# Kernel tuning notes

Hardware: AMD Instinct MI355X
Metric: run time of the kernel (lower is better)

Reference implementation:

```python
import jax, jax.numpy as jnp
import numpy as np

N_NODES = 100000
NUM_REL = 2


def rgcn_conv(x, src, dst, etype, W, root, bias):
    """PyG-style RGCNConv: per-relation mean aggregation + root transform + bias.
    x: [N, in], W: [R, in, out], root: [in, out], bias: [out].
    """
    R = W.shape[0]
    N = x.shape[0]
    # Pre-transform nodes by every relation weight: [R, N, out]
    xr = jnp.einsum('ni,rio->rno', x, W)
    msgs = xr[etype, src]  # [E, out] gather per-edge, relation-typed
    seg_id = dst * R + etype  # combined (node, relation) segment id
    summed = jax.ops.segment_sum(msgs, seg_id, num_segments=N * R)
    cnt = jax.ops.segment_sum(jnp.ones(etype.shape, x.dtype), seg_id, num_segments=N * R)
    summed = summed.reshape(N, R, -1)
    cnt = cnt.reshape(N, R, 1)
    agg = (summed / jnp.maximum(cnt, 1.0)).sum(axis=1)  # sum over relations of per-relation means
    return agg + x @ root + bias


def setup_inputs() -> dict:
    key = jax.random.key(0)
    ks = jax.random.split(key, 9)
    d = 128
    E = 800000
    sc = 1.0 / np.sqrt(d)
    return {
        'x': jax.random.normal(ks[0], (N_NODES, d), jnp.float32),
        'edge_index_a': jax.random.randint(ks[1], (2, E), 0, N_NODES, jnp.int64),
        'edge_index_b': jax.random.randint(ks[2], (2, E), 0, N_NODES, jnp.int64),
        'W1': jax.random.normal(ks[3], (NUM_REL, d, d), jnp.float32) * sc,
        'root1': jax.random.normal(ks[4], (d, d), jnp.float32) * sc,
        'b1': jnp.zeros((d,), jnp.float32),
        'W2': jax.random.normal(ks[5], (NUM_REL, d, d), jnp.float32) * sc,
        'root2': jax.random.normal(ks[6], (d, d), jnp.float32) * sc,
        'b2': jnp.zeros((d,), jnp.float32),
    }


def reference(x, edge_index_a, edge_index_b, W1, root1, b1, W2, root2, b2):
    # Concatenate per-relation edge lists + build edge_type ids (a->0, b->1)
    edge_index = jnp.concatenate([edge_index_a, edge_index_b], axis=1)
    etype = jnp.concatenate([
        jnp.zeros((edge_index_a.shape[1],), jnp.int32),
        jnp.ones((edge_index_b.shape[1],), jnp.int32),
    ])
    src, dst = edge_index[0], edge_index[1]
    h = rgcn_conv(x, src, dst, etype, W1, root1, b1)
    h = jax.nn.relu(h)
    out = rgcn_conv(h, src, dst, etype, W2, root2, b2)
    return out
```

## Files before the change

kernel.cpp:

```cpp
#include <hip/hip_runtime.h>
#include <hip/hip_bf16.h>


typedef __attribute__((ext_vector_type(8))) short bf16x8;
typedef __attribute__((ext_vector_type(4))) float f32x4;
typedef unsigned short ushort_t;
typedef unsigned int uint_t;

#define BSHIFT 9
#define SEGB (1 << (BSHIFT + 1))
#define NBMAX 256
#define SLAB 16384
#define CH_PER_THREAD 8
#define CHUNK (256 * CH_PER_THREAD)

#define GBM 256
#define KCH 128
#define LDBE 136

#define ROWB 768
#define XOFF 512

__device__ __forceinline__ ushort_t f2b(float f) {
  union { float f; uint_t u; } v;
  v.f = f;
  uint_t u = v.u;
  return (ushort_t)((u + 0x7FFFu + ((u >> 16) & 1u)) >> 16);
}
__device__ __forceinline__ void dot2acc(float& a, uint_t pk, uint_t sel) {
  asm("v_dot2_f32_bf16 %0, %1, %2, %0" : "+v"(a) : "v"(pk), "v"(sel));
}

__global__ __launch_bounds__(256) void prep(
    const float* __restrict__ W1, const float* __restrict__ root1,
    const float* __restrict__ W2, const float* __restrict__ root2,
    ushort_t* __restrict__ Bt1, ushort_t* __restrict__ Bt2,
    const float* __restrict__ x, ushort_t* __restrict__ aggbuf1, int N) {
  int b = blockIdx.x;
  if (b < 384) {
    int flat = b * 256 + threadIdx.x;
    int which = flat >= 49152;
    int idx = flat - which * 49152;
    int c = idx / 384;
    int k = idx - c * 384;
    const float* W = which ? W2 : W1;
    const float* root = which ? root2 : root1;
    ushort_t* Bt = which ? Bt2 : Bt1;
    float v = (k < 256) ? W[(size_t)k * 128 + c] : root[(size_t)(k - 256) * 128 + c];
    Bt[(size_t)c * 384 + k] = f2b(v);
  } else {
    int idx = (b - 384) * 256 + threadIdx.x;
    int n = idx >> 6, lane = idx & 63;
    if (n < N) {
      float2 v = *(const float2*)(x + (size_t)n * 128 + lane * 2);
      uint_t pk = (uint_t)f2b(v.x) | ((uint_t)f2b(v.y) << 16);
      *(uint_t*)(aggbuf1 + (size_t)n * 384 + 256 + lane * 2) = pk;
    }
  }
}

__global__ __launch_bounds__(256) void bucket_bin(
    const int* __restrict__ ea, const int* __restrict__ eb,
    int E, int NB, int* __restrict__ cursor, uint_t* __restrict__ staging) {
  __shared__ int h[NBMAX];
  __shared__ int bbase[NBMAX];
  __shared__ int lofs[NBMAX];
  __shared__ int sscan[256];
  __shared__ uint_t sval[CHUNK];
  __shared__ int sdst[CHUNK];
  int t = threadIdx.x;
  for (int i = t; i < NB; i += 256) h[i] = 0;
  __syncthreads();

  int tbase = blockIdx.x * CHUNK + t;
  int total = 2 * E;
  uint_t val[CH_PER_THREAD];
  short bktv[CH_PER_THREAD];
#pragma unroll
  for (int j = 0; j < CH_PER_THREAD; ++j) {
    int i = tbase + j * 256;
    if (i < total) {
      int src, dst, rel;
      if (i < E) { src = ea[i];     dst = ea[E + i]; rel = 0; }
      else       { src = eb[i - E]; dst = eb[i];     rel = 1; }
      int seg = dst * 2 + rel;
      int bkt = seg >> (BSHIFT + 1);
      val[j] = ((uint_t)src << 10) | (uint_t)(seg & (SEGB - 1));
      bktv[j] = (short)bkt;
      atomicAdd(&h[bkt], 1);
    } else {
      bktv[j] = -1;
    }
  }
  __syncthreads();
  {
    int v = (t < NB) ? h[t] : 0;
    sscan[t] = v;
    __syncthreads();
    for (int off = 1; off < 256; off <<= 1) {
      int tmp = (t >= off) ? sscan[t - off] : 0;
      __syncthreads();
      sscan[t] += tmp;
      __syncthreads();
    }
    if (t < NB) {
      lofs[t] = sscan[t] - v;
      bbase[t] = v ? t * SLAB + atomicAdd(&cursor[t], v) : 0;
    }
  }
  __syncthreads();
  for (int i = t; i < NB; i += 256) h[i] = 0;
  __syncthreads();
#pragma unroll
  for (int j = 0; j < CH_PER_THREAD; ++j) {
    if (bktv[j] >= 0) {
      int bkt = bktv[j];
      int r = atomicAdd(&h[bkt], 1);
      int pos = lofs[bkt] + r;
      sval[pos] = val[j];
      sdst[pos] = bbase[bkt] + r;
    }
  }
  __syncthreads();
  int nrec = total - blockIdx.x * CHUNK;
  if (nrec > CHUNK) nrec = CHUNK;
  for (int i = t; i < nrec; i += 256)
    staging[sdst[i]] = sval[i];
}

__global__ __launch_bounds__(256) void bucket_build(
    const uint_t* __restrict__ staging, const int* __restrict__ cursor,
    int* __restrict__ csr, int* __restrict__ offs,
    int* __restrict__ ends, int nseg) {
  __shared__ int scnt[SEGB];
  __shared__ int sexcl[SEGB];
  __shared__ int sdata[256];
  int b = blockIdx.x;
  int t = threadIdx.x;
  int base = b * SLAB;
  int ne = cursor[b];
  int seg0 = b << (BSHIFT + 1);

  for (int i = t; i < SEGB; i += 256) scnt[i] = 0;
  __syncthreads();
  const uint_t* st = staging + base;
  for (int i = t; i < ne; i += 256) {
    atomicAdd(&scnt[st[i] & (SEGB - 1)], 1);
  }
  __syncthreads();
  int c0 = scnt[t * 4 + 0], c1 = scnt[t * 4 + 1];
  int c2 = scnt[t * 4 + 2], c3 = scnt[t * 4 + 3];
  int s = c0 + c1 + c2 + c3;
  sdata[t] = s;
  __syncthreads();
  for (int off = 1; off < 256; off <<= 1) {
    int tmp = (t >= off) ? sdata[t - off] : 0;
    __syncthreads();
    sdata[t] += tmp;
    __syncthreads();
  }
  int excl = sdata[t] - s;
  int e0 = excl, e1 = excl + c0, e2 = e1 + c1, e3 = e2 + c2;
  sexcl[t * 4 + 0] = e0;
  sexcl[t * 4 + 1] = e1;
  sexcl[t * 4 + 2] = e2;
  sexcl[t * 4 + 3] = e3;
  {
    int g = seg0 + t * 4;
    if (g + 0 < nseg) { offs[g + 0] = base + e0; ends[g + 0] = base + e0 + c0; }
    if (g + 1 < nseg) { offs[g + 1] = base + e1; ends[g + 1] = base + e1 + c1; }
    if (g + 2 < nseg) { offs[g + 2] = base + e2; ends[g + 2] = base + e2 + c2; }
    if (g + 3 < nseg) { offs[g + 3] = base + e3; ends[g + 3] = base + e3 + c3; }
  }
  scnt[t * 4 + 0] = 0;
  scnt[t * 4 + 1] = 0;
  scnt[t * 4 + 2] = 0;
  scnt[t * 4 + 3] = 0;
  __syncthreads();
  for (int i = t; i < ne; i += 256) {
    uint_t rec = st[i];
    int seg = (int)(rec & (SEGB - 1));
    int src = (int)(rec >> 10);
    int r = atomicAdd(&scnt[seg], 1);
    csr[base + sexcl[seg] + r] = src * ROWB + XOFF;
  }
}

__global__ __launch_bounds__(256) void agg_kernel(
    const char* __restrict__ xbc,
    const int* __restrict__ csr,
    const int* __restrict__ offs, const int* __restrict__ ends,
    ushort_t* __restrict__ agg, int nseg) {
  int wid = (blockIdx.x * blockDim.x + threadIdx.x) >> 6;
  if (wid >= nseg) return;
  int lane = threadIdx.x & 63;
  int q = lane >> 4;
  int t = lane & 15;
  int beg = offs[wid], end = ends[wid];
  const uint_t sel_lo = 0x00003F80u;
  const uint_t sel_hi = 0x3F800000u;

  float acc[8];
#pragma unroll
  for (int j = 0; j < 8; ++j) acc[j] = 0.f;

  const char* xt = xbc + t * 16;
  int e = beg + q;
  for (; e + 4 < end; e += 8) {
    int o0 = csr[e];
    int o1 = csr[e + 4];
    uint4 v0 = *(const uint4*)(xt + o0);
    uint4 v1 = *(const uint4*)(xt + o1);
    dot2acc(acc[0], v0.x, sel_lo); dot2acc(acc[1], v0.x, sel_hi);
    dot2acc(acc[2], v0.y, sel_lo); dot2acc(acc[3], v0.y, sel_hi);
    dot2acc(acc[4], v0.z, sel_lo); dot2acc(acc[5], v0.z, sel_hi);
    dot2acc(acc[6], v0.w, sel_lo); dot2acc(acc[7], v0.w, sel_hi);
    dot2acc(acc[0], v1.x, sel_lo); dot2acc(acc[1], v1.x, sel_hi);
    dot2acc(acc[2], v1.y, sel_lo); dot2acc(acc[3], v1.y, sel_hi);
    dot2acc(acc[4], v1.z, sel_lo); dot2acc(acc[5], v1.z, sel_hi);
    dot2acc(acc[6], v1.w, sel_lo); dot2acc(acc[7], v1.w, sel_hi);
  }
  if (e < end) {
    int o0 = csr[e];
    uint4 v0 = *(const uint4*)(xt + o0);
    dot2acc(acc[0], v0.x, sel_lo); dot2acc(acc[1], v0.x, sel_hi);
    dot2acc(acc[2], v0.y, sel_lo); dot2acc(acc[3], v0.y, sel_hi);
    dot2acc(acc[4], v0.z, sel_lo); dot2acc(acc[5], v0.z, sel_hi);
    dot2acc(acc[6], v0.w, sel_lo); dot2acc(acc[7], v0.w, sel_hi);
  }

#pragma unroll
  for (int j = 0; j < 8; ++j) {
    acc[j] += __shfl_xor(acc[j], 16);
    acc[j] += __shfl_xor(acc[j], 32);
  }

  int c = end - beg;
  float inv = 1.0f / (float)(c > 1 ? c : 1);
  if (q == 0) {
    uint4 o;
    o.x = (uint_t)f2b(acc[0] * inv) | ((uint_t)f2b(acc[1] * inv) << 16);
    o.y = (uint_t)f2b(acc[2] * inv) | ((uint_t)f2b(acc[3] * inv) << 16);
    o.z = (uint_t)f2b(acc[4] * inv) | ((uint_t)f2b(acc[5] * inv) << 16);
    o.w = (uint_t)f2b(acc[6] * inv) | ((uint_t)f2b(acc[7] * inv) << 16);
    int n = wid >> 1, r = wid & 1;
    *(uint4*)(agg + (size_t)n * 384 + r * 128 + t * 8) = o;
  }
}

__device__ __forceinline__ void do_mfma32(
    const char* bs, f32x4 (&acc)[4][8], const bf16x8 (&a)[4],
    int ks, int lrow, int kg) {
  bf16x8 b[8];
#pragma unroll
  for (int c = 0; c < 8; ++c)
    b[c] = *(const bf16x8*)(bs + (c * 16 + lrow) * (LDBE * 2) +
                            (ks * 4 + kg) * 16);
#pragma unroll
  for (int r = 0; r < 4; ++r)
#pragma unroll
    for (int c = 0; c < 8; ++c)
      acc[r][c] = __builtin_amdgcn_mfma_f32_16x16x32_bf16(a[r], b[c], acc[r][c], 0, 0, 0);
}

template <int MODE>
__global__ __launch_bounds__(256, 2) void mfma_gemm(
    const ushort_t* __restrict__ A,
    const ushort_t* __restrict__ Bt,
    const float* __restrict__ bias,
    float* __restrict__ outf,
    ushort_t* __restrict__ outb,
    int M) {
  __shared__ __align__(16) ushort_t Bs[2][128 * LDBE];
  const int tid = threadIdx.x;
  const int lane = tid & 63;
  const int wave = tid >> 6;
  const int lrow = lane & 15;
  const int kg = lane >> 4;
  const int rowbase = blockIdx.x * GBM + wave * 64;

  f32x4 acc[4][8];
#pragma unroll
  for (int r = 0; r < 4; ++r)
#pragma unroll
    for (int c = 0; c < 8; ++c) acc[r][c] = (f32x4){0.f, 0.f, 0.f, 0.f};

  uint4 stg[8];
#pragma unroll
  for (int j = 0; j < 8; ++j) {
    int flat = tid + j * 256;
    int col = flat >> 4;
    int q = flat & 15;
    stg[j] = *(const uint4*)(Bt + (size_t)col * 384 + q * 8);
  }
#pragma unroll
  for (int j = 0; j < 8; ++j) {
    int flat = tid + j * 256;
    int col = flat >> 4;
    int q = flat & 15;
    *(uint4*)((char*)&Bs[0][0] + col * (LDBE * 2) + q * 16) = stg[j];
  }
  __syncthreads();

  int cur = 0;
  for (int ch = 0; ch < 3; ++ch) {
    if (ch < 2) {
#pragma unroll
      for (int j = 0; j < 8; ++j) {
        int flat = tid + j * 256;
        int col = flat >> 4;
        int q = flat & 15;
        stg[j] = *(const uint4*)(Bt + (size_t)col * 384 + (ch + 1) * KCH + q * 8);
      }
    }
    const ushort_t* ab = A + (size_t)ch * KCH + kg * 8;
    const char* bsbase = (const char*)&Bs[0][0] + cur * (128 * LDBE * 2);
    bf16x8 aA[4], aB[4];
#pragma unroll
    for (int r = 0; r < 4; ++r)
      aA[r] = *(const bf16x8*)(ab + (size_t)(rowbase + r * 16 + lrow) * 384);
#pragma unroll
    for (int r = 0; r < 4; ++r)
      aB[r] = *(const bf16x8*)(ab + (size_t)(rowbase + r * 16 + lrow) * 384 + 32);
    do_mfma32(bsbase, acc, aA, 0, lrow, kg);
#pragma unroll
    for (int r = 0; r < 4; ++r)
      aA[r] = *(const bf16x8*)(ab + (size_t)(rowbase + r * 16 + lrow) * 384 + 64);
    do_mfma32(bsbase, acc, aB, 1, lrow, kg);
#pragma unroll
    for (int r = 0; r < 4; ++r)
      aB[r] = *(const bf16x8*)(ab + (size_t)(rowbase + r * 16 + lrow) * 384 + 96);
    do_mfma32(bsbase, acc, aA, 2, lrow, kg);
    do_mfma32(bsbase, acc, aB, 3, lrow, kg);
    if (ch < 2) {
#pragma unroll
      for (int j = 0; j < 8; ++j) {
        int flat = tid + j * 256;
        int col = flat >> 4;
        int q = flat & 15;
        *(uint4*)((char*)&Bs[0][0] + (cur ^ 1) * (128 * LDBE * 2) +
                  col * (LDBE * 2) + q * 16) = stg[j];
      }
      __syncthreads();
      cur ^= 1;
    }
  }

  if (MODE == 1) {
    __syncthreads();
    ushort_t* ws = (ushort_t*)&Bs[0][0] + wave * (64 * 128);
#pragma unroll
    for (int c = 0; c < 8; ++c) {
      int col = c * 16 + lrow;
      float bv = bias[col];
#pragma unroll
      for (int r = 0; r < 4; ++r)
#pragma unroll
        for (int j = 0; j < 4; ++j) {
          float v = fmaxf(acc[r][c][j] + bv, 0.f);
          ws[(r * 16 + kg * 4 + j) * 128 + col] = f2b(v);
        }
    }
    __syncthreads();
#pragma unroll
    for (int rr = 0; rr < 16; ++rr) {
      int lr = rr * 4 + (lane >> 4);
      int row = rowbase + lr;
      int tq = lane & 15;
      if (row < M) {
        uint4 v = *(const uint4*)(ws + lr * 128 + tq * 8);
        *(uint4*)(outb + (size_t)row * 384 + 256 + tq * 8) = v;
      }
    }
  } else {
#pragma unroll
    for (int c = 0; c < 8; ++c) {
      int col = c * 16 + lrow;
      float bv = bias[col];
#pragma unroll
      for (int r = 0; r < 4; ++r) {
        int r0 = rowbase + r * 16 + kg * 4;
#pragma unroll
        for (int j = 0; j < 4; ++j) {
          int row = r0 + j;
          if (row < M) {
            outf[(size_t)row * 128 + col] = acc[r][c][j] + bv;
          }
        }
      }
    }
  }
}

extern "C" void kernel_launch(void* const* d_in, const int* in_sizes, int n_in,
                              void* d_out, int out_size, void* d_ws, size_t ws_size,
                              hipStream_t stream) {
  const float* x     = (const float*)d_in[0];
  const int*   ea    = (const int*)d_in[1];
  const int*   eb    = (const int*)d_in[2];
  const float* W1    = (const float*)d_in[3];
  const float* root1 = (const float*)d_in[4];
  const float* b1    = (const float*)d_in[5];
  const float* W2    = (const float*)d_in[6];
  const float* root2 = (const float*)d_in[7];
  const float* b2    = (const float*)d_in[8];
  float* out = (float*)d_out;

  const int N = in_sizes[0] / 128;
  const int E = in_sizes[1] / 2;
  const int nseg = N * 2;
  const int Mblk = (N + GBM - 1) / GBM;
  const int Mpad = Mblk * GBM;
  const int NB = ((N - 1) >> BSHIFT) + 1;
  const int nchunk = (2 * E + CHUNK - 1) / CHUNK;
  const int XSB = (N * 64 + 255) / 256;

  char* p = (char*)d_ws;
  ushort_t* aggbuf1 = (ushort_t*)p;  p += (size_t)Mpad * 384 * sizeof(ushort_t);
  ushort_t* aggbuf2 = (ushort_t*)p;  p += (size_t)Mpad * 384 * sizeof(ushort_t);
  ushort_t* Bt1 = (ushort_t*)p;      p += (size_t)128 * 384 * sizeof(ushort_t);
  ushort_t* Bt2 = (ushort_t*)p;      p += (size_t)128 * 384 * sizeof(ushort_t);
  int* csr = (int*)p;                p += (size_t)NBMAX * SLAB * sizeof(int);
  int* offs = (int*)p;               p += (size_t)nseg * sizeof(int);
  int* ends = (int*)p;               p += (size_t)nseg * sizeof(int);
  int* cursor = (int*)p;             p += NBMAX * sizeof(int);
  uint_t* staging = (uint_t*)aggbuf2;

  hipMemsetAsync(cursor, 0, NBMAX * sizeof(int), stream);

  prep<<<384 + XSB, 256, 0, stream>>>(
      W1, root1, W2, root2, Bt1, Bt2, x, aggbuf1, N);

  bucket_bin<<<nchunk, 256, 0, stream>>>(ea, eb, E, NB, cursor, staging);
  bucket_build<<<NB, 256, 0, stream>>>(staging, cursor, csr, offs, ends, nseg);

  const int agg_blocks = (nseg + 3) / 4;

  agg_kernel<<<agg_blocks, 256, 0, stream>>>((const char*)aggbuf1, csr, offs,
                                             ends, aggbuf1, nseg);
  mfma_gemm<1><<<Mblk, 256, 0, stream>>>(aggbuf1, Bt1, b1, nullptr, aggbuf2, N);

  agg_kernel<<<agg_blocks, 256, 0, stream>>>((const char*)aggbuf2, csr, offs,
                                             ends, aggbuf2, nseg);
  mfma_gemm<0><<<Mblk, 256, 0, stream>>>(aggbuf2, Bt2, b2, out, nullptr, N);
}
```

Baseline: 308.0 us.

## Fuse edge binning into prep kernel and widen bucket_build to 1024 threads

```diff
diff --git a/kernel.cpp b/kernel.cpp
--- a/kernel.cpp
+++ b/kernel.cpp
@@ -31,14 +31,81 @@
   asm("v_dot2_f32_bf16 %0, %1, %2, %0" : "+v"(a) : "v"(pk), "v"(sel));
 }
 
-__global__ __launch_bounds__(256) void prep(
+__global__ __launch_bounds__(256) void prep_bin(
+    const int* __restrict__ ea, const int* __restrict__ eb, int E, int NB,
+    int* __restrict__ cursor, uint_t* __restrict__ staging, int nchunk,
     const float* __restrict__ W1, const float* __restrict__ root1,
     const float* __restrict__ W2, const float* __restrict__ root2,
     ushort_t* __restrict__ Bt1, ushort_t* __restrict__ Bt2,
     const float* __restrict__ x, ushort_t* __restrict__ aggbuf1, int N) {
+  __shared__ int h[NBMAX];
+  __shared__ int bbase[NBMAX];
+  __shared__ int lofs[NBMAX];
+  __shared__ int sscan[256];
+  __shared__ uint_t sval[CHUNK];
+  __shared__ int sdst[CHUNK];
   int b = blockIdx.x;
-  if (b < 384) {
-    int flat = b * 256 + threadIdx.x;
+  int t = threadIdx.x;
+
+  if (b < nchunk) {
+    for (int i = t; i < NB; i += 256) h[i] = 0;
+    __syncthreads();
+    int tbase = b * CHUNK + t;
+    int total = 2 * E;
+    uint_t val[CH_PER_THREAD];
+    short bktv[CH_PER_THREAD];
+#pragma unroll
+    for (int j = 0; j < CH_PER_THREAD; ++j) {
+      int i = tbase + j * 256;
+      if (i < total) {
+        int src, dst, rel;
+        if (i < E) { src = ea[i];     dst = ea[E + i]; rel = 0; }
+        else       { src = eb[i - E]; dst = eb[i];     rel = 1; }
+        int seg = dst * 2 + rel;
+        int bkt = seg >> (BSHIFT + 1);
+        val[j] = ((uint_t)src << 10) | (uint_t)(seg & (SEGB - 1));
+        bktv[j] = (short)bkt;
+        atomicAdd(&h[bkt], 1);
+      } else {
+        bktv[j] = -1;
+      }
+    }
+    __syncthreads();
+    {
+      int v = (t < NB) ? h[t] : 0;
+      sscan[t] = v;
+      __syncthreads();
+      for (int off = 1; off < 256; off <<= 1) {
+        int tmp = (t >= off) ? sscan[t - off] : 0;
+        __syncthreads();
+        sscan[t] += tmp;
+        __syncthreads();
+      }
+      if (t < NB) {
+        lofs[t] = sscan[t] - v;
+        bbase[t] = v ? t * SLAB + atomicAdd(&cursor[t], v) : 0;
+      }
+    }
+    __syncthreads();
+    for (int i = t; i < NB; i += 256) h[i] = 0;
+    __syncthreads();
+#pragma unroll
+    for (int j = 0; j < CH_PER_THREAD; ++j) {
+      if (bktv[j] >= 0) {
+        int bkt = bktv[j];
+        int r = atomicAdd(&h[bkt], 1);
+        int pos = lofs[bkt] + r;
+        sval[pos] = val[j];
+        sdst[pos] = bbase[bkt] + r;
+      }
+    }
+    __syncthreads();
+    int nrec = 2 * E - b * CHUNK;
+    if (nrec > CHUNK) nrec = CHUNK;
+    for (int i = t; i < nrec; i += 256)
+      staging[sdst[i]] = sval[i];
+  } else if (b < nchunk + 384) {
+    int flat = (b - nchunk) * 256 + t;
     int which = flat >= 49152;
     int idx = flat - which * 49152;
     int c = idx / 384;
@@ -49,7 +116,7 @@
     float v = (k < 256) ? W[(size_t)k * 128 + c] : root[(size_t)(k - 256) * 128 + c];
     Bt[(size_t)c * 384 + k] = f2b(v);
   } else {
-    int idx = (b - 384) * 256 + threadIdx.x;
+    int idx = (b - nchunk - 384) * 256 + t;
     int n = idx >> 6, lane = idx & 63;
     if (n < N) {
       float2 v = *(const float2*)(x + (size_t)n * 128 + lane * 2);
@@ -59,125 +126,43 @@
   }
 }
 
-__global__ __launch_bounds__(256) void bucket_bin(
-    const int* __restrict__ ea, const int* __restrict__ eb,
-    int E, int NB, int* __restrict__ cursor, uint_t* __restrict__ staging) {
-  __shared__ int h[NBMAX];
-  __shared__ int bbase[NBMAX];
-  __shared__ int lofs[NBMAX];
-  __shared__ int sscan[256];
-  __shared__ uint_t sval[CHUNK];
-  __shared__ int sdst[CHUNK];
-  int t = threadIdx.x;
-  for (int i = t; i < NB; i += 256) h[i] = 0;
-  __syncthreads();
-
-  int tbase = blockIdx.x * CHUNK + t;
-  int total = 2 * E;
-  uint_t val[CH_PER_THREAD];
-  short bktv[CH_PER_THREAD];
-#pragma unroll
-  for (int j = 0; j < CH_PER_THREAD; ++j) {
-    int i = tbase + j * 256;
-    if (i < total) {
-      int src, dst, rel;
-      if (i < E) { src = ea[i];     dst = ea[E + i]; rel = 0; }
-      else       { src = eb[i - E]; dst = eb[i];     rel = 1; }
-      int seg = dst * 2 + rel;
-      int bkt = seg >> (BSHIFT + 1);
-      val[j] = ((uint_t)src << 10) | (uint_t)(seg & (SEGB - 1));
-      bktv[j] = (short)bkt;
-      atomicAdd(&h[bkt], 1);
-    } else {
-      bktv[j] = -1;
-    }
-  }
-  __syncthreads();
-  {
-    int v = (t < NB) ? h[t] : 0;
-    sscan[t] = v;
-    __syncthreads();
-    for (int off = 1; off < 256; off <<= 1) {
-      int tmp = (t >= off) ? sscan[t - off] : 0;
-      __syncthreads();
-      sscan[t] += tmp;
-      __syncthreads();
-    }
-    if (t < NB) {
-      lofs[t] = sscan[t] - v;
-      bbase[t] = v ? t * SLAB + atomicAdd(&cursor[t], v) : 0;
-    }
-  }
-  __syncthreads();
-  for (int i = t; i < NB; i += 256) h[i] = 0;
-  __syncthreads();
-#pragma unroll
-  for (int j = 0; j < CH_PER_THREAD; ++j) {
-    if (bktv[j] >= 0) {
-      int bkt = bktv[j];
-      int r = atomicAdd(&h[bkt], 1);
-      int pos = lofs[bkt] + r;
-      sval[pos] = val[j];
-      sdst[pos] = bbase[bkt] + r;
-    }
-  }
-  __syncthreads();
-  int nrec = total - blockIdx.x * CHUNK;
-  if (nrec > CHUNK) nrec = CHUNK;
-  for (int i = t; i < nrec; i += 256)
-    staging[sdst[i]] = sval[i];
-}
-
-__global__ __launch_bounds__(256) void bucket_build(
+__global__ __launch_bounds__(1024) void bucket_build(
     const uint_t* __restrict__ staging, const int* __restrict__ cursor,
     int* __restrict__ csr, int* __restrict__ offs,
     int* __restrict__ ends, int nseg) {
   __shared__ int scnt[SEGB];
   __shared__ int sexcl[SEGB];
-  __shared__ int sdata[256];
+  __shared__ int sdata[SEGB];
   int b = blockIdx.x;
   int t = threadIdx.x;
   int base = b * SLAB;
   int ne = cursor[b];
   int seg0 = b << (BSHIFT + 1);
 
-  for (int i = t; i < SEGB; i += 256) scnt[i] = 0;
+  scnt[t] = 0;
   __syncthreads();
   const uint_t* st = staging + base;
-  for (int i = t; i < ne; i += 256) {
+  for (int i = t; i < ne; i += 1024)
     atomicAdd(&scnt[st[i] & (SEGB - 1)], 1);
-  }
   __syncthreads();
-  int c0 = scnt[t * 4 + 0], c1 = scnt[t * 4 + 1];
-  int c2 = scnt[t * 4 + 2], c3 = scnt[t * 4 + 3];
-  int s = c0 + c1 + c2 + c3;
-  sdata[t] = s;
+  int c = scnt[t];
+  sdata[t] = c;
   __syncthreads();
-  for (int off = 1; off < 256; off <<= 1) {
+  for (int off = 1; off < 1024; off <<= 1) {
     int tmp = (t >= off) ? sdata[t - off] : 0;
     __syncthreads();
     sdata[t] += tmp;
     __syncthreads();
   }
-  int excl = sdata[t] - s;
-  int e0 = excl, e1 = excl + c0, e2 = e1 + c1, e3 = e2 + c2;
-  sexcl[t * 4 + 0] = e0;
-  sexcl[t * 4 + 1] = e1;
-  sexcl[t * 4 + 2] = e2;
-  sexcl[t * 4 + 3] = e3;
+  int excl = sdata[t] - c;
+  sexcl[t] = excl;
   {
-    int g = seg0 + t * 4;
-    if (g + 0 < nseg) { offs[g + 0] = base + e0; ends[g + 0] = base + e0 + c0; }
-    if (g + 1 < nseg) { offs[g + 1] = base + e1; ends[g + 1] = base + e1 + c1; }
-    if (g + 2 < nseg) { offs[g + 2] = base + e2; ends[g + 2] = base + e2 + c2; }
-    if (g + 3 < nseg) { offs[g + 3] = base + e3; ends[g + 3] = base + e3 + c3; }
-  }
-  scnt[t * 4 + 0] = 0;
-  scnt[t * 4 + 1] = 0;
-  scnt[t * 4 + 2] = 0;
-  scnt[t * 4 + 3] = 0;
+    int g = seg0 + t;
+    if (g < nseg) { offs[g] = base + excl; ends[g] = base + excl + c; }
+  }
+  scnt[t] = 0;
   __syncthreads();
-  for (int i = t; i < ne; i += 256) {
+  for (int i = t; i < ne; i += 1024) {
     uint_t rec = st[i];
     int seg = (int)(rec & (SEGB - 1));
     int src = (int)(rec >> 10);
@@ -428,11 +413,11 @@
 
   hipMemsetAsync(cursor, 0, NBMAX * sizeof(int), stream);
 
-  prep<<<384 + XSB, 256, 0, stream>>>(
+  prep_bin<<<nchunk + 384 + XSB, 256, 0, stream>>>(
+      ea, eb, E, NB, cursor, staging, nchunk,
       W1, root1, W2, root2, Bt1, Bt2, x, aggbuf1, N);
 
-  bucket_bin<<<nchunk, 256, 0, stream>>>(ea, eb, E, NB, cursor, staging);
-  bucket_build<<<NB, 256, 0, stream>>>(staging, cursor, csr, offs, ends, nseg);
+  bucket_build<<<NB, 1024, 0, stream>>>(staging, cursor, csr, offs, ends, nseg);
 
   const int agg_blocks = (nseg + 3) / 4;
 
```

Result: faster. 299.3 us (-2.8%).
